# Kernel tuning notes

Measured on AMD Instinct MI355X. Metric: run time of the kernel, lower is better.

Reference implementation:

```python
import jax, jax.numpy as jnp
import numpy as np

B, S, H = 1, 2048, 768
NH, HD, NF = 12, 64, 128
ALPHA = 0.9
SIGMA = 1.0
EPS_NORM = 1e-5


def setup_inputs() -> dict:
    key = jax.random.key(0)
    ks = jax.random.split(key, 12)
    s = 1.0 / np.sqrt(H)
    inp = {
        "hidden_states": jax.random.normal(ks[0], (B, S, H), dtype=jnp.float32),
        "attention_mask": jnp.ones((B, 1, 1, S), dtype=jnp.float32),
        "Wq": jax.random.normal(ks[1], (H, H), dtype=jnp.float32) * s,
        "bq": jnp.zeros((H,), dtype=jnp.float32),
        "Wk": jax.random.normal(ks[2], (H, H), dtype=jnp.float32) * s,
        "bk": jnp.zeros((H,), dtype=jnp.float32),
        "Wv": jax.random.normal(ks[3], (H, H), dtype=jnp.float32) * s,
        "bv": jnp.zeros((H,), dtype=jnp.float32),
        "Wo": jax.random.normal(ks[4], (H, H), dtype=jnp.float32) * s,
        "bo": jnp.zeros((H,), dtype=jnp.float32),
        # per-head RFF params: omega ~ N(0, I), bias ~ U[0, 2pi]
        "omega": jax.random.normal(ks[5], (NH, NF, HD), dtype=jnp.float32),
        "rff_b": jax.random.uniform(ks[6], (NH, NF), dtype=jnp.float32, maxval=2.0 * np.pi),
    }
    return inp


def _phi(x, omega, rff_b):
    # x: (b, h, s, d) -> RFF features (b, h, s, f)
    z = jnp.einsum("bhsd,hfd->bhsf", x, omega) / SIGMA + rff_b[None, :, None, :]
    phi = jnp.sqrt(2.0 / NF) * jnp.cos(z)
    # normalize=True: L2-normalize feature vectors
    phi = phi / (jnp.linalg.norm(phi, axis=-1, keepdims=True) + 1e-6)
    return phi


def reference(hidden_states, attention_mask, Wq, bq, Wk, bk, Wv, bv, Wo, bo, omega, rff_b):
    b, s, _ = hidden_states.shape

    def proj(W, bias):
        y = jnp.einsum("bsh,oh->bso", hidden_states, W) + bias
        return y.reshape(b, s, NH, HD).transpose(0, 2, 1, 3)  # (b,h,s,d)

    q = proj(Wq, bq)
    k = proj(Wk, bk)
    v = proj(Wv, bv)

    dot_scores = jnp.einsum("bhsd,bhtd->bhst", q, k) / jnp.sqrt(jnp.float32(HD))

    qn = q / (jnp.linalg.norm(q, axis=-1, keepdims=True) + EPS_NORM)
    kn = k / (jnp.linalg.norm(k, axis=-1, keepdims=True) + EPS_NORM)
    phi_q = _phi(qn, omega, rff_b)
    phi_k = _phi(kn, omega, rff_b)
    kernel_scores = jnp.einsum("bhsf,bhtf->bhst", phi_q, phi_k)

    scores = ALPHA * dot_scores + (1.0 - ALPHA) * kernel_scores
    scores = scores + (attention_mask - 1.0) * 10000.0

    weights = jax.nn.softmax(scores, axis=-1)  # dropout is identity in eval
    context = jnp.einsum("bhst,bhtd->bhsd", weights, v)
    context = context.transpose(0, 2, 1, 3).reshape(b, s, H)
    output = jnp.einsum("bsh,oh->bso", context, Wo) + bo
    return output, weights
```

## Files before the change

### kernel.cpp

```cpp
#include <hip/hip_runtime.h>
#include <cmath>

#define TS 2048
#define TH 768
#define TNH 12
#define THD 64
#define TNF 128
#define KC 192

typedef __attribute__((ext_vector_type(4))) short s16x4;
typedef __attribute__((ext_vector_type(8))) short short8;
typedef __attribute__((ext_vector_type(8))) __bf16 bf16x8;
typedef __attribute__((ext_vector_type(4))) float floatx4;

__device__ __forceinline__ short f2bf(float x) {
    union { float f; unsigned u; } v; v.f = x;
    unsigned r = v.u + 0x7FFFu + ((v.u >> 16) & 1u);
    return (short)(r >> 16);
}
__device__ __forceinline__ float bf2f(short x) {
    union { unsigned u; float f; } v;
    v.u = ((unsigned)(unsigned short)x) << 16;
    return v.f;
}

__device__ __forceinline__ float waveReduceSum(float v) {
#pragma unroll
    for (int off = 32; off >= 1; off >>= 1) v += __shfl_xor(v, off, 64);
    return v;
}
__device__ __forceinline__ float waveReduceMax(float v) {
#pragma unroll
    for (int off = 32; off >= 1; off >>= 1) v = fmaxf(v, __shfl_xor(v, off, 64));
    return v;
}

__global__ __launch_bounds__(256) void k_cvt_bf16(
    const float* __restrict__ s0, const float* __restrict__ s1,
    const float* __restrict__ s2, const float* __restrict__ s3,
    const float* __restrict__ s4, const float* __restrict__ s5,
    short* __restrict__ d0, short* __restrict__ d1,
    short* __restrict__ d2, short* __restrict__ d3,
    short* __restrict__ d4, short* __restrict__ d5) {
    const int y = blockIdx.y;
    const float* srcs[6] = {s0, s1, s2, s3, s4, s5};
    short* dsts[6] = {d0, d1, d2, d3, d4, d5};
    const int n4s[6] = {TS * TH / 4, TH * TH / 4, TH * TH / 4, TH * TH / 4,
                        TH * TH / 4, TNH * TNF * THD / 4};
    const float* src = srcs[y];
    short* dst = dsts[y];
    const int n4 = n4s[y];
    for (int i = blockIdx.x * 256 + threadIdx.x; i < n4; i += gridDim.x * 256) {
        float4 v = ((const float4*)src)[i];
        s16x4 o;
        o[0] = f2bf(v.x); o[1] = f2bf(v.y); o[2] = f2bf(v.z); o[3] = f2bf(v.w);
        *(s16x4*)&dst[i * 4] = o;
    }
}

__global__ __launch_bounds__(256) void k_proj_qkv_mfma(
    const short* __restrict__ Xb,
    const short* __restrict__ Wqb, const short* __restrict__ Wkb, const short* __restrict__ Wvb,
    const float* __restrict__ b0, const float* __restrict__ b1, const float* __restrict__ b2,
    float* __restrict__ invq, float* __restrict__ invk, short* __restrict__ Vb,
    short* __restrict__ Qc, short* __restrict__ Kc) {
    __shared__ __align__(16) short Asb[128][40];
    __shared__ __align__(16) short Bsb[128][40];
    const int z = blockIdx.z;
    const short* W = (z == 0) ? Wqb : ((z == 1) ? Wkb : Wvb);
    const float* bias = (z == 0) ? b0 : ((z == 1) ? b1 : b2);
    const int n0 = blockIdx.x * 128;
    const int m0 = blockIdx.y * 128;
    const int tid = threadIdx.x;
    const int lane = tid & 63;
    const int w = tid >> 6;
    const int wm = (w >> 1) * 64, wn = (w & 1) * 64;
    const int fr = lane & 15;
    const int quad = lane >> 4;

    floatx4 acc[4][4] = {};

    for (int k0 = 0; k0 < TH; k0 += 32) {
#pragma unroll
        for (int l = 0; l < 2; ++l) {
            int c = tid + l * 256;
            int row = c >> 2, col = (c & 3) << 3;
            *(short8*)&Asb[row][col] = *(const short8*)&Xb[(size_t)(m0 + row) * TH + k0 + col];
            *(short8*)&Bsb[row][col] = *(const short8*)&W[(size_t)(n0 + row) * TH + k0 + col];
        }
        __syncthreads();
        bf16x8 af[4], bfr[4];
#pragma unroll
        for (int i = 0; i < 4; ++i) af[i] = *(const bf16x8*)&Asb[wm + i * 16 + fr][quad * 8];
#pragma unroll
        for (int j = 0; j < 4; ++j) bfr[j] = *(const bf16x8*)&Bsb[wn + j * 16 + fr][quad * 8];
#pragma unroll
        for (int i = 0; i < 4; ++i)
#pragma unroll
            for (int j = 0; j < 4; ++j)
                acc[i][j] = __builtin_amdgcn_mfma_f32_16x16x32_bf16(af[i], bfr[j], acc[i][j], 0, 0, 0);
        __syncthreads();
    }
    if (z == 2) {
#pragma unroll
        for (int j = 0; j < 4; ++j) {
            int n = n0 + wn + j * 16 + fr;
            int h = n >> 6, d = n & 63;
            float bv = bias[n];
#pragma unroll
            for (int i = 0; i < 4; ++i) {
                int t = m0 + wm + i * 16 + quad * 4;
                s16x4 pk;
#pragma unroll
                for (int r = 0; r < 4; ++r) pk[r] = f2bf(acc[i][j][r] + bv);
                *(s16x4*)&Vb[(size_t)(h * THD + d) * TS + t] = pk;
            }
        }
    } else {
        short* cc = z ? Kc : Qc;
        float* invd = z ? invk : invq;
        const float qs = z ? 1.0f : 0.1125f;
        const int hh = (n0 + wn) >> 6;
        float ssr[4][4] = {};
#pragma unroll
        for (int j = 0; j < 4; ++j) {
            int n = n0 + wn + j * 16 + fr;
            int d = n & 63;
            float bv = bias[n];
#pragma unroll
            for (int i = 0; i < 4; ++i) {
#pragma unroll
                for (int r = 0; r < 4; ++r) {
                    int m = m0 + wm + i * 16 + quad * 4 + r;
                    float val = acc[i][j][r] + bv;
                    cc[(size_t)(hh * TS + m) * KC + d] = f2bf(val * qs);
                    ssr[i][r] += val * val;
                }
            }
        }
#pragma unroll
        for (int i = 0; i < 4; ++i)
#pragma unroll
            for (int r = 0; r < 4; ++r) {
                float ss = ssr[i][r];
#pragma unroll
                for (int off = 1; off <= 8; off <<= 1) ss += __shfl_xor(ss, off, 64);
                if (fr == 0) {
                    int m = m0 + wm + i * 16 + quad * 4 + r;
                    invd[hh * TS + m] = 1.0f / (qs * (sqrtf(ss) + 1e-5f));
                }
            }
    }
}

__global__ __launch_bounds__(256) void k_proj_out_mfma(
    const short* __restrict__ ctxb, const short* __restrict__ Wob,
    const float* __restrict__ bias, float* __restrict__ out) {
    __shared__ __align__(16) short Asb[128][40];
    __shared__ __align__(16) short Bsb[128][40];
    const int n0 = blockIdx.x * 128;
    const int m0 = blockIdx.y * 128;
    const int tid = threadIdx.x;
    const int lane = tid & 63;
    const int w = tid >> 6;
    const int wm = (w >> 1) * 64, wn = (w & 1) * 64;
    const int fr = lane & 15;
    const int quad = lane >> 4;

    floatx4 acc[4][4] = {};

    for (int k0 = 0; k0 < TH; k0 += 32) {
#pragma unroll
        for (int l = 0; l < 2; ++l) {
            int c = tid + l * 256;
            int row = c >> 2, col = (c & 3) << 3;
            *(short8*)&Asb[row][col] = *(const short8*)&ctxb[(size_t)(m0 + row) * TH + k0 + col];
            *(short8*)&Bsb[row][col] = *(const short8*)&Wob[(size_t)(n0 + row) * TH + k0 + col];
        }
        __syncthreads();
        bf16x8 af[4], bfr[4];
#pragma unroll
        for (int i = 0; i < 4; ++i) af[i] = *(const bf16x8*)&Asb[wm + i * 16 + fr][quad * 8];
#pragma unroll
        for (int j = 0; j < 4; ++j) bfr[j] = *(const bf16x8*)&Bsb[wn + j * 16 + fr][quad * 8];
#pragma unroll
        for (int i = 0; i < 4; ++i)
#pragma unroll
            for (int j = 0; j < 4; ++j)
                acc[i][j] = __builtin_amdgcn_mfma_f32_16x16x32_bf16(af[i], bfr[j], acc[i][j], 0, 0, 0);
        __syncthreads();
    }
#pragma unroll
    for (int j = 0; j < 4; ++j) {
        int n = n0 + wn + j * 16 + fr;
        float bv = bias[n];
#pragma unroll
        for (int i = 0; i < 4; ++i)
#pragma unroll
            for (int r = 0; r < 4; ++r) {
                int m = m0 + wm + i * 16 + quad * 4 + r;
                out[(size_t)m * TH + n] = acc[i][j][r] + bv;
            }
    }
}

__global__ __launch_bounds__(256) void k_phi_mfma(
    const float* __restrict__ invq, const float* __restrict__ invk,
    const short* __restrict__ omegab, const float* __restrict__ rffb,
    short* __restrict__ Qc, short* __restrict__ Kc) {
    __shared__ __align__(16) short Asb[128][40];
    __shared__ __align__(16) short Bsb[128][40];
    __shared__ float smP[4][64];
    const int z = blockIdx.y;
    const int h = z >> 1, which = z & 1;
    const float* inv = which ? invk : invq;
    short* buf = which ? Kc : Qc;
    const int m0 = blockIdx.x * 128;
    const int tid = threadIdx.x;
    const int lane = tid & 63;
    const int w = tid >> 6;
    const int wm = (w >> 1) * 64, wn = (w & 1) * 64;
    const int fr = lane & 15;
    const int quad = lane >> 4;

    floatx4 acc[4][4] = {};

    for (int k0 = 0; k0 < THD; k0 += 32) {
#pragma unroll
        for (int l = 0; l < 2; ++l) {
            int c = tid + l * 256;
            int row = c >> 2, col = (c & 3) << 3;
            int rq = h * TS + m0 + row;
            float s = inv[rq];
            short8 a = *(const short8*)&buf[(size_t)rq * KC + k0 + col];
            short8 o;
#pragma unroll
            for (int e = 0; e < 8; ++e) o[e] = f2bf(bf2f(a[e]) * s);
            *(short8*)&Asb[row][col] = o;
            *(short8*)&Bsb[row][col] = *(const short8*)&omegab[(size_t)(h * TNF + row) * THD + k0 + col];
        }
        __syncthreads();
        bf16x8 af[4], bfr[4];
#pragma unroll
        for (int i = 0; i < 4; ++i) af[i] = *(const bf16x8*)&Asb[wm + i * 16 + fr][quad * 8];
#pragma unroll
        for (int j = 0; j < 4; ++j) bfr[j] = *(const bf16x8*)&Bsb[wn + j * 16 + fr][quad * 8];
#pragma unroll
        for (int i = 0; i < 4; ++i)
#pragma unroll
            for (int j = 0; j < 4; ++j)
                acc[i][j] = __builtin_amdgcn_mfma_f32_16x16x32_bf16(af[i], bfr[j], acc[i][j], 0, 0, 0);
        __syncthreads();
    }
    float bvj[4];
#pragma unroll
    for (int j = 0; j < 4; ++j) bvj[j] = rffb[h * TNF + wn + j * 16 + fr];
    float ssr[4][4] = {};
#pragma unroll
    for (int i = 0; i < 4; ++i)
#pragma unroll
        for (int j = 0; j < 4; ++j)
#pragma unroll
            for (int r = 0; r < 4; ++r) {
                float p = 0.125f * cosf(acc[i][j][r] + bvj[j]);
                acc[i][j][r] = p;
                ssr[i][r] += p * p;
            }
#pragma unroll
    for (int i = 0; i < 4; ++i)
#pragma unroll
        for (int r = 0; r < 4; ++r) {
#pragma unroll
            for (int off = 1; off <= 8; off <<= 1) ssr[i][r] += __shfl_xor(ssr[i][r], off, 64);
        }
    if (fr == 0) {
#pragma unroll
        for (int i = 0; i < 4; ++i)
#pragma unroll
            for (int r = 0; r < 4; ++r) smP[w][i * 16 + quad * 4 + r] = ssr[i][r];
    }
    __syncthreads();
    const float scale0 = which ? 1.0f : 0.1f;
#pragma unroll
    for (int i = 0; i < 4; ++i)
#pragma unroll
        for (int r = 0; r < 4; ++r) {
            int rl = i * 16 + quad * 4 + r;
            float ss = smP[w][rl] + smP[w ^ 1][rl];
            float sc = scale0 / (sqrtf(ss) + 1e-6f);
            int m = m0 + wm + rl;
#pragma unroll
            for (int j = 0; j < 4; ++j) {
                int f = wn + j * 16 + fr;
                buf[(size_t)(h * TS + m) * KC + 64 + f] = f2bf(acc[i][j][r] * sc);
            }
        }
}

__global__ __launch_bounds__(256) void k_scores_mfma(
    const short* __restrict__ Qc, const short* __restrict__ Kc,
    const float* __restrict__ mask, float* __restrict__ wout) {
    __shared__ __align__(16) short Asb[128][40];
    __shared__ __align__(16) short Bsb[128][40];
    const int h = blockIdx.z;
    const int n0 = blockIdx.x * 128;
    const int m0 = blockIdx.y * 128;
    const int tid = threadIdx.x;
    const int lane = tid & 63;
    const int w = tid >> 6;
    const int wm = (w >> 1) * 64, wn = (w & 1) * 64;
    const int fr = lane & 15;
    const int quad = lane >> 4;

    floatx4 acc[4][4] = {};

    for (int k0 = 0; k0 < KC; k0 += 32) {
#pragma unroll
        for (int l = 0; l < 2; ++l) {
            int c = tid + l * 256;
            int row = c >> 2, col = (c & 3) << 3;
            short8 a = *(const short8*)&Qc[(size_t)(h * TS + m0 + row) * KC + k0 + col];
            *(short8*)&Asb[row][col] = a;
            short8 b = *(const short8*)&Kc[(size_t)(h * TS + n0 + row) * KC + k0 + col];
            *(short8*)&Bsb[row][col] = b;
        }
        __syncthreads();
        bf16x8 af[4], bfr[4];
#pragma unroll
        for (int i = 0; i < 4; ++i) af[i] = *(const bf16x8*)&Asb[wm + i * 16 + fr][quad * 8];
#pragma unroll
        for (int j = 0; j < 4; ++j) bfr[j] = *(const bf16x8*)&Bsb[wn + j * 16 + fr][quad * 8];
#pragma unroll
        for (int i = 0; i < 4; ++i)
#pragma unroll
            for (int j = 0; j < 4; ++j)
                acc[i][j] = __builtin_amdgcn_mfma_f32_16x16x32_bf16(af[i], bfr[j], acc[i][j], 0, 0, 0);
        __syncthreads();
    }
#pragma unroll
    for (int j = 0; j < 4; ++j) {
        int col_g = n0 + wn + j * 16 + fr;
        float mb = (mask[col_g] - 1.0f) * 10000.0f;
#pragma unroll
        for (int i = 0; i < 4; ++i) {
#pragma unroll
            for (int r = 0; r < 4; ++r) {
                int row_g = m0 + wm + i * 16 + quad * 4 + r;
                wout[(size_t)(h * TS + row_g) * TS + col_g] = acc[i][j][r] + mb;
            }
        }
    }
}

__global__ __launch_bounds__(256) void k_softmax(float* __restrict__ wout) {
    const int row = blockIdx.x;
    float4* p = (float4*)(wout + (size_t)row * TS);
    const int tid = threadIdx.x;
    float4 x0 = p[tid], x1 = p[tid + 256];
    float mx = fmaxf(fmaxf(fmaxf(x0.x, x0.y), fmaxf(x0.z, x0.w)),
                     fmaxf(fmaxf(x1.x, x1.y), fmaxf(x1.z, x1.w)));
    mx = waveReduceMax(mx);
    __shared__ float rm[4];
    __shared__ float rs[4];
    if ((tid & 63) == 0) rm[tid >> 6] = mx;
    __syncthreads();
    mx = fmaxf(fmaxf(rm[0], rm[1]), fmaxf(rm[2], rm[3]));
    float e[8];
    e[0] = __expf(x0.x - mx); e[1] = __expf(x0.y - mx);
    e[2] = __expf(x0.z - mx); e[3] = __expf(x0.w - mx);
    e[4] = __expf(x1.x - mx); e[5] = __expf(x1.y - mx);
    e[6] = __expf(x1.z - mx); e[7] = __expf(x1.w - mx);
    float sum = ((e[0] + e[1]) + (e[2] + e[3])) + ((e[4] + e[5]) + (e[6] + e[7]));
    sum = waveReduceSum(sum);
    if ((tid & 63) == 0) rs[tid >> 6] = sum;
    __syncthreads();
    sum = rs[0] + rs[1] + rs[2] + rs[3];
    float rinv = 1.0f / sum;
    x0.x = e[0] * rinv; x0.y = e[1] * rinv; x0.z = e[2] * rinv; x0.w = e[3] * rinv;
    x1.x = e[4] * rinv; x1.y = e[5] * rinv; x1.z = e[6] * rinv; x1.w = e[7] * rinv;
    p[tid] = x0;
    p[tid + 256] = x1;
}

__global__ __launch_bounds__(256) void k_ctx_mfma(
    const float* __restrict__ wout, const short* __restrict__ Vb, short* __restrict__ ctxb) {
    __shared__ __align__(16) short Asb[128][40];
    __shared__ __align__(16) short Bsb[64][40];
    const int h = blockIdx.y;
    const int m0 = blockIdx.x * 128;
    const int tid = threadIdx.x;
    const int lane = tid & 63;
    const int w = tid >> 6;
    const int wm = w * 32;
    const int fr = lane & 15;
    const int quad = lane >> 4;
    floatx4 acc[2][4] = {};
    for (int k0 = 0; k0 < TS; k0 += 32) {
#pragma unroll
        for (int l = 0; l < 4; ++l) {
            int idx = tid + l * 256;
            int row = idx >> 3, col = (idx & 7) << 2;
            float4 a = *(const float4*)&wout[(size_t)(h * TS + m0 + row) * TS + k0 + col];
            s16x4 s;
            s[0] = f2bf(a.x); s[1] = f2bf(a.y); s[2] = f2bf(a.z); s[3] = f2bf(a.w);
            *(s16x4*)&Asb[row][col] = s;
        }
        {
            int row = tid >> 2, col = (tid & 3) << 3;
            *(short8*)&Bsb[row][col] =
                *(const short8*)&Vb[(size_t)(h * THD + row) * TS + k0 + col];
        }
        __syncthreads();
        bf16x8 af[2], bfr[4];
#pragma unroll
        for (int i = 0; i < 2; ++i) af[i] = *(const bf16x8*)&Asb[wm + i * 16 + fr][quad * 8];
#pragma unroll
        for (int j = 0; j < 4; ++j) bfr[j] = *(const bf16x8*)&Bsb[j * 16 + fr][quad * 8];
#pragma unroll
        for (int i = 0; i < 2; ++i)
#pragma unroll
            for (int j = 0; j < 4; ++j)
                acc[i][j] = __builtin_amdgcn_mfma_f32_16x16x32_bf16(af[i], bfr[j], acc[i][j], 0, 0, 0);
        __syncthreads();
    }
#pragma unroll
    for (int i = 0; i < 2; ++i)
#pragma unroll
        for (int j = 0; j < 4; ++j)
#pragma unroll
            for (int r = 0; r < 4; ++r) {
                int row_g = m0 + wm + i * 16 + quad * 4 + r;
                ctxb[(size_t)row_g * TH + h * THD + j * 16 + fr] = f2bf(acc[i][j][r]);
            }
}

extern "C" void kernel_launch(void* const* d_in, const int* in_sizes, int n_in,
                              void* d_out, int out_size, void* d_ws, size_t ws_size,
                              hipStream_t stream) {
    const float* hs    = (const float*)d_in[0];
    const float* mask  = (const float*)d_in[1];
    const float* Wq    = (const float*)d_in[2];
    const float* bq    = (const float*)d_in[3];
    const float* Wk    = (const float*)d_in[4];
    const float* bk    = (const float*)d_in[5];
    const float* Wv    = (const float*)d_in[6];
    const float* bv    = (const float*)d_in[7];
    const float* Wo    = (const float*)d_in[8];
    const float* bo    = (const float*)d_in[9];
    const float* omega = (const float*)d_in[10];
    const float* rffb  = (const float*)d_in[11];

    float* out0 = (float*)d_out;
    float* wout = out0 + TS * TH;

    float* ws   = (float*)d_ws;
    short* Vb   = (short*)(ws + 3145728);
    short* Wob  = (short*)(ws + 3932160);
    short* omegab = (short*)(ws + 4227072);
    float* invq = ws + 4718592;
    float* invk = ws + 4743168;
    short* ctxb = (short*)(ws + 4767744);
    short* Qc   = (short*)(ws + 6340608);
    short* Kc   = (short*)(ws + 8699904);

    short* Xb  = (short*)wout;
    short* Wqb = Xb + (size_t)TS * TH;
    short* Wkb = Wqb + (size_t)TH * TH;
    short* Wvb = Wkb + (size_t)TH * TH;

    k_cvt_bf16<<<dim3(512, 6), 256, 0, stream>>>(hs, Wq, Wk, Wv, Wo, omega,
                                                 Xb, Wqb, Wkb, Wvb, Wob, omegab);
    k_proj_qkv_mfma<<<dim3(6, 16, 3), 256, 0, stream>>>(Xb, Wqb, Wkb, Wvb, bq, bk, bv,
                                                        invq, invk, Vb, Qc, Kc);
    k_phi_mfma<<<dim3(16, 24), 256, 0, stream>>>(invq, invk, omegab, rffb, Qc, Kc);
    k_scores_mfma<<<dim3(16, 16, 12), 256, 0, stream>>>(Qc, Kc, mask, wout);
    k_softmax<<<TNH * TS, 256, 0, stream>>>(wout);
    k_ctx_mfma<<<dim3(16, 12), 256, 0, stream>>>(wout, Vb, ctxb);
    k_proj_out_mfma<<<dim3(6, 16), 256, 0, stream>>>(ctxb, Wob, bo, out0);
}
```

Before: 489.0 us.

## Fuse softmax into score and context kernels via atomic row sums

```diff
diff --git a/kernel.cpp b/kernel.cpp
--- a/kernel.cpp
+++ b/kernel.cpp
@@ -24,25 +24,20 @@
     return v.f;
 }
 
-__device__ __forceinline__ float waveReduceSum(float v) {
-#pragma unroll
-    for (int off = 32; off >= 1; off >>= 1) v += __shfl_xor(v, off, 64);
-    return v;
-}
-__device__ __forceinline__ float waveReduceMax(float v) {
-#pragma unroll
-    for (int off = 32; off >= 1; off >>= 1) v = fmaxf(v, __shfl_xor(v, off, 64));
-    return v;
-}
-
 __global__ __launch_bounds__(256) void k_cvt_bf16(
     const float* __restrict__ s0, const float* __restrict__ s1,
     const float* __restrict__ s2, const float* __restrict__ s3,
     const float* __restrict__ s4, const float* __restrict__ s5,
     short* __restrict__ d0, short* __restrict__ d1,
     short* __restrict__ d2, short* __restrict__ d3,
-    short* __restrict__ d4, short* __restrict__ d5) {
+    short* __restrict__ d4, short* __restrict__ d5,
+    float* __restrict__ rowsum) {
     const int y = blockIdx.y;
+    if (y == 6) {
+        for (int i = blockIdx.x * 256 + threadIdx.x; i < TNH * TS / 4; i += gridDim.x * 256)
+            ((float4*)rowsum)[i] = (float4){0.f, 0.f, 0.f, 0.f};
+        return;
+    }
     const float* srcs[6] = {s0, s1, s2, s3, s4, s5};
     short* dsts[6] = {d0, d1, d2, d3, d4, d5};
     const int n4s[6] = {TS * TH / 4, TH * TH / 4, TH * TH / 4, TH * TH / 4,
@@ -299,7 +294,7 @@
 
 __global__ __launch_bounds__(256) void k_scores_mfma(
     const short* __restrict__ Qc, const short* __restrict__ Kc,
-    const float* __restrict__ mask, float* __restrict__ wout) {
+    const float* __restrict__ mask, float* __restrict__ wout, float* __restrict__ rowsum) {
     __shared__ __align__(16) short Asb[128][40];
     __shared__ __align__(16) short Bsb[128][40];
     const int h = blockIdx.z;
@@ -337,55 +332,42 @@
                 acc[i][j] = __builtin_amdgcn_mfma_f32_16x16x32_bf16(af[i], bfr[j], acc[i][j], 0, 0, 0);
         __syncthreads();
     }
+    float mb[4];
+#pragma unroll
+    for (int j = 0; j < 4; ++j) mb[j] = (mask[n0 + wn + j * 16 + fr] - 1.0f) * 10000.0f;
+    float psum[4][4] = {};
 #pragma unroll
     for (int j = 0; j < 4; ++j) {
         int col_g = n0 + wn + j * 16 + fr;
-        float mb = (mask[col_g] - 1.0f) * 10000.0f;
 #pragma unroll
         for (int i = 0; i < 4; ++i) {
 #pragma unroll
             for (int r = 0; r < 4; ++r) {
                 int row_g = m0 + wm + i * 16 + quad * 4 + r;
-                wout[(size_t)(h * TS + row_g) * TS + col_g] = acc[i][j][r] + mb;
-            }
-        }
-    }
-}
-
-__global__ __launch_bounds__(256) void k_softmax(float* __restrict__ wout) {
-    const int row = blockIdx.x;
-    float4* p = (float4*)(wout + (size_t)row * TS);
-    const int tid = threadIdx.x;
-    float4 x0 = p[tid], x1 = p[tid + 256];
-    float mx = fmaxf(fmaxf(fmaxf(x0.x, x0.y), fmaxf(x0.z, x0.w)),
-                     fmaxf(fmaxf(x1.x, x1.y), fmaxf(x1.z, x1.w)));
-    mx = waveReduceMax(mx);
-    __shared__ float rm[4];
-    __shared__ float rs[4];
-    if ((tid & 63) == 0) rm[tid >> 6] = mx;
-    __syncthreads();
-    mx = fmaxf(fmaxf(rm[0], rm[1]), fmaxf(rm[2], rm[3]));
-    float e[8];
-    e[0] = __expf(x0.x - mx); e[1] = __expf(x0.y - mx);
-    e[2] = __expf(x0.z - mx); e[3] = __expf(x0.w - mx);
-    e[4] = __expf(x1.x - mx); e[5] = __expf(x1.y - mx);
-    e[6] = __expf(x1.z - mx); e[7] = __expf(x1.w - mx);
-    float sum = ((e[0] + e[1]) + (e[2] + e[3])) + ((e[4] + e[5]) + (e[6] + e[7]));
-    sum = waveReduceSum(sum);
-    if ((tid & 63) == 0) rs[tid >> 6] = sum;
-    __syncthreads();
-    sum = rs[0] + rs[1] + rs[2] + rs[3];
-    float rinv = 1.0f / sum;
-    x0.x = e[0] * rinv; x0.y = e[1] * rinv; x0.z = e[2] * rinv; x0.w = e[3] * rinv;
-    x1.x = e[4] * rinv; x1.y = e[5] * rinv; x1.z = e[6] * rinv; x1.w = e[7] * rinv;
-    p[tid] = x0;
-    p[tid + 256] = x1;
+                float e = __expf(acc[i][j][r] + mb[j]);
+                wout[(size_t)(h * TS + row_g) * TS + col_g] = e;
+                psum[i][r] += e;
+            }
+        }
+    }
+#pragma unroll
+    for (int i = 0; i < 4; ++i)
+#pragma unroll
+        for (int r = 0; r < 4; ++r) {
+            float p = psum[i][r];
+#pragma unroll
+            for (int off = 1; off <= 8; off <<= 1) p += __shfl_xor(p, off, 64);
+            if (fr == 0)
+                atomicAdd(&rowsum[h * TS + m0 + wm + i * 16 + quad * 4 + r], p);
+        }
 }
 
 __global__ __launch_bounds__(256) void k_ctx_mfma(
-    const float* __restrict__ wout, const short* __restrict__ Vb, short* __restrict__ ctxb) {
+    float* __restrict__ wout, const float* __restrict__ rowsum,
+    const short* __restrict__ Vb, short* __restrict__ ctxb) {
     __shared__ __align__(16) short Asb[128][40];
     __shared__ __align__(16) short Bsb[64][40];
+    __shared__ float smR[128];
     const int h = blockIdx.y;
     const int m0 = blockIdx.x * 128;
     const int tid = threadIdx.x;
@@ -394,15 +376,21 @@
     const int wm = w * 32;
     const int fr = lane & 15;
     const int quad = lane >> 4;
+    if (tid < 128) smR[tid] = 1.0f / rowsum[h * TS + m0 + tid];
+    __syncthreads();
     floatx4 acc[2][4] = {};
     for (int k0 = 0; k0 < TS; k0 += 32) {
 #pragma unroll
         for (int l = 0; l < 4; ++l) {
             int idx = tid + l * 256;
             int row = idx >> 3, col = (idx & 7) << 2;
-            float4 a = *(const float4*)&wout[(size_t)(h * TS + m0 + row) * TS + k0 + col];
+            float rin = smR[row];
+            size_t base = (size_t)(h * TS + m0 + row) * TS + k0 + col;
+            float4 a = *(const float4*)&wout[base];
+            float w0 = a.x * rin, w1 = a.y * rin, w2 = a.z * rin, w3 = a.w * rin;
+            *(float4*)&wout[base] = (float4){w0, w1, w2, w3};
             s16x4 s;
-            s[0] = f2bf(a.x); s[1] = f2bf(a.y); s[2] = f2bf(a.z); s[3] = f2bf(a.w);
+            s[0] = f2bf(w0); s[1] = f2bf(w1); s[2] = f2bf(w2); s[3] = f2bf(w3);
             *(s16x4*)&Asb[row][col] = s;
         }
         {
@@ -454,6 +442,7 @@
     float* wout = out0 + TS * TH;
 
     float* ws   = (float*)d_ws;
+    float* rowsum = ws;
     short* Vb   = (short*)(ws + 3145728);
     short* Wob  = (short*)(ws + 3932160);
     short* omegab = (short*)(ws + 4227072);
@@ -468,13 +457,12 @@
     short* Wkb = Wqb + (size_t)TH * TH;
     short* Wvb = Wkb + (size_t)TH * TH;
 
-    k_cvt_bf16<<<dim3(512, 6), 256, 0, stream>>>(hs, Wq, Wk, Wv, Wo, omega,
-                                                 Xb, Wqb, Wkb, Wvb, Wob, omegab);
+    k_cvt_bf16<<<dim3(512, 7), 256, 0, stream>>>(hs, Wq, Wk, Wv, Wo, omega,
+                                                 Xb, Wqb, Wkb, Wvb, Wob, omegab, rowsum);
     k_proj_qkv_mfma<<<dim3(6, 16, 3), 256, 0, stream>>>(Xb, Wqb, Wkb, Wvb, bq, bk, bv,
                                                         invq, invk, Vb, Qc, Kc);
     k_phi_mfma<<<dim3(16, 24), 256, 0, stream>>>(invq, invk, omegab, rffb, Qc, Kc);
-    k_scores_mfma<<<dim3(16, 16, 12), 256, 0, stream>>>(Qc, Kc, mask, wout);
-    k_softmax<<<TNH * TS, 256, 0, stream>>>(wout);
-    k_ctx_mfma<<<dim3(16, 12), 256, 0, stream>>>(wout, Vb, ctxb);
+    k_scores_mfma<<<dim3(16, 16, 12), 256, 0, stream>>>(Qc, Kc, mask, wout, rowsum);
+    k_ctx_mfma<<<dim3(16, 12), 256, 0, stream>>>(wout, rowsum, Vb, ctxb);
     k_proj_out_mfma<<<dim3(6, 16), 256, 0, stream>>>(ctxb, Wob, bo, out0);
 }
```

After: 558.1 us. 14.1% more time.
